# Optimization experiments

Measured on AMD Instinct MI355X. Metric: run time of the kernel, lower is better.

Reference implementation:

```python
import jax, jax.numpy as jnp
import numpy as np

B, H, W, C, HEADS = 32, 56, 56, 384, 12
WIN = (7, 7)
SHIFT = (3, 3)
N = WIN[0] * WIN[1]
HD = C // HEADS
HIDDEN = int(C * 2.0)
CPB_HIDDEN = 512


def _cpb_tables():
    # log-spaced continuous relative coordinates table (SwinV2 CPB)
    coords = [np.arange(-(w - 1), w, dtype=np.float32) for w in WIN]
    g = np.stack(np.meshgrid(*coords, indexing='ij'))
    for i, w in enumerate(WIN):
        g[i] = g[i] / (w - 1)
    rel = np.moveaxis(g, 0, -1)[None]              # (1, 2w0-1, 2w1-1, 2)
    rel = 8.0 * rel
    rel = np.sign(rel) * np.log2(np.abs(rel) + 1.0) / np.log2(8.0)
    grid = np.stack(np.meshgrid(*[np.arange(w) for w in WIN], indexing='ij')).reshape(2, -1)
    dists = grid[:, :, None] - grid[:, None, :]    # (2, N, N)
    dists[0] = (dists[0] + WIN[0] - 1) * (2 * WIN[1] - 1)
    dists[1] = (dists[1] + WIN[1] - 1)
    return jnp.asarray(rel, jnp.float32), jnp.asarray(dists.sum(0), jnp.int32)

REL_TAB, RPB_IDX = _cpb_tables()


def _compute_mask():
    img = np.zeros((1, H, W, 1), np.float32)
    cnt = 0
    for s0 in (slice(0, -WIN[0]), slice(-WIN[0], -SHIFT[0]), slice(-SHIFT[0], None)):
        for s1 in (slice(0, -WIN[1]), slice(-WIN[1], -SHIFT[1]), slice(-SHIFT[1], None)):
            img[:, s0, s1, :] = cnt
            cnt += 1
    w = img.reshape(1, H // WIN[0], WIN[0], W // WIN[1], WIN[1], 1)
    w = w.transpose(0, 1, 3, 2, 4, 5).reshape(-1, N)
    m = w[:, None, :] - w[:, :, None]
    return jnp.asarray(np.where(m != 0, -100.0, 0.0).astype(np.float32))


def _layernorm(x, g, b, eps=1e-5):
    mu = x.mean(-1, keepdims=True)
    var = ((x - mu) ** 2).mean(-1, keepdims=True)
    return (x - mu) / jnp.sqrt(var + eps) * g + b


def _window_partition(x):
    b = x.shape[0]
    x = x.reshape(b, H // WIN[0], WIN[0], W // WIN[1], WIN[1], C)
    return x.transpose(0, 1, 3, 2, 4, 5).reshape(-1, N, C)


def _window_reverse(win):
    x = win.reshape(B, H // WIN[0], W // WIN[1], WIN[0], WIN[1], C)
    return x.transpose(0, 1, 3, 2, 4, 5).reshape(B, H, W, C)


def setup_inputs() -> dict:
    key = jax.random.key(0)
    ks = jax.random.split(key, 16)
    s = 0.02
    return {
        'x': jax.random.normal(ks[0], (B, H, W, C), jnp.float32),
        'attn_mask': _compute_mask(),                              # (nW, N, N)
        'norm1_g': jnp.ones((C,), jnp.float32),
        'norm1_b': jnp.zeros((C,), jnp.float32),
        'qkv_w': jax.random.normal(ks[1], (3 * C, C), jnp.float32) * s,
        'qkv_b': jnp.zeros((3 * C,), jnp.float32),
        'proj_w': jax.random.normal(ks[2], (C, C), jnp.float32) * s,
        'proj_b': jnp.zeros((C,), jnp.float32),
        'cpb_w1': jax.random.normal(ks[3], (CPB_HIDDEN, 2), jnp.float32) * s,
        'cpb_b1': jnp.zeros((CPB_HIDDEN,), jnp.float32),
        'cpb_w2': jax.random.normal(ks[4], (HEADS, CPB_HIDDEN), jnp.float32) * s,
        'logit_scale': jnp.full((HEADS, 1, 1), np.log(10.0), jnp.float32),
        'norm2_g': jnp.ones((C,), jnp.float32),
        'norm2_b': jnp.zeros((C,), jnp.float32),
        'mlp_w1': jax.random.normal(ks[5], (HIDDEN, C), jnp.float32) * s,
        'mlp_b1': jnp.zeros((HIDDEN,), jnp.float32),
        'mlp_w2': jax.random.normal(ks[6], (C, HIDDEN), jnp.float32) * s,
        'mlp_b2': jnp.zeros((C,), jnp.float32),
    }


def reference(x, attn_mask, norm1_g, norm1_b, qkv_w, qkv_b, proj_w, proj_b,
              cpb_w1, cpb_b1, cpb_w2, logit_scale, norm2_g, norm2_b,
              mlp_w1, mlp_b1, mlp_w2, mlp_b2):
    # continuous position bias: MLP over log-spaced rel coords, gathered per pair
    h = jax.nn.relu(REL_TAB @ cpb_w1.T + cpb_b1)       # (1, 2w0-1, 2w1-1, 512)
    tab = (h @ cpb_w2.T).reshape(-1, HEADS)            # ((2w0-1)*(2w1-1), heads)
    rpb = tab[RPB_IDX.reshape(-1)].reshape(N, N, HEADS)
    rpb = 16.0 * jax.nn.sigmoid(rpb)
    rpb = rpb.transpose(2, 0, 1)                       # (heads, N, N)

    shortcut = x
    xn = _layernorm(x, norm1_g, norm1_b)
    xs = jnp.roll(xn, (-SHIFT[0], -SHIFT[1]), axis=(1, 2))
    wnd = _window_partition(xs)                        # (B*nW, N, C)
    qkv = (wnd @ qkv_w.T + qkv_b).reshape(-1, N, 3, HEADS, HD)
    q = qkv[:, :, 0].transpose(0, 2, 1, 3)             # (B*nW, heads, N, hd)
    k = qkv[:, :, 1].transpose(0, 2, 1, 3)
    v = qkv[:, :, 2].transpose(0, 2, 1, 3)
    qn = q / jnp.maximum(jnp.linalg.norm(q, axis=-1, keepdims=True), 1e-12)
    kn = k / jnp.maximum(jnp.linalg.norm(k, axis=-1, keepdims=True), 1e-12)
    scale = jnp.exp(jnp.minimum(logit_scale, jnp.log(100.0)))   # (heads,1,1)
    attn = jnp.einsum('bhnd,bhmd->bhnm', qn, kn) * scale + rpb
    nW = attn_mask.shape[0]
    attn = attn.reshape(B, nW, HEADS, N, N) + attn_mask[None, :, None]
    attn = jax.nn.softmax(attn.reshape(-1, HEADS, N, N), axis=-1)
    o = jnp.einsum('bhnm,bhmd->bhnd', attn, v)
    o = o.transpose(0, 2, 1, 3).reshape(-1, N, C)
    o = o @ proj_w.T + proj_b
    xr = _window_reverse(o)
    xr = jnp.roll(xr, (SHIFT[0], SHIFT[1]), axis=(1, 2))
    x = shortcut + xr
    xm = _layernorm(x, norm2_g, norm2_b)
    xm = jax.nn.gelu(xm @ mlp_w1.T + mlp_b1, approximate=False) @ mlp_w2.T + mlp_b2
    return x + xm
```

## Files before the change

kernel.cpp:

```cpp
#include <hip/hip_runtime.h>
#include <stdint.h>

typedef unsigned short u16;
typedef __bf16 bf16x8 __attribute__((ext_vector_type(8)));
typedef float f32x4 __attribute__((ext_vector_type(4)));

__device__ __forceinline__ float b2f(u16 u) {
    union { float f; uint32_t i; } x; x.i = ((uint32_t)u) << 16; return x.f;
}
__device__ __forceinline__ u16 f2b(float f) {
    union { float f; uint32_t i; } x; x.f = f;
    uint32_t r = (x.i + 0x7fffu + ((x.i >> 16) & 1u)) >> 16;
    return (u16)r;
}

__global__ __launch_bounds__(512)
void cpb_tab_kernel(const float* __restrict__ w1, const float* __restrict__ b1,
                    const float* __restrict__ w2, float* __restrict__ tab) {
    __shared__ float hbuf[512];
    int p = blockIdx.x, j = threadIdx.x;
    int i0 = p / 13, i1 = p % 13;
    float c0 = (i0 - 6) * (8.0f / 6.0f), c1 = (i1 - 6) * (8.0f / 6.0f);
    float r0 = copysignf(log2f(fabsf(c0) + 1.0f) * (1.0f / 3.0f), c0);
    float r1 = copysignf(log2f(fabsf(c1) + 1.0f) * (1.0f / 3.0f), c1);
    float h = r0 * w1[j * 2] + r1 * w1[j * 2 + 1] + b1[j];
    hbuf[j] = fmaxf(h, 0.0f);
    __syncthreads();
    if (j < 12) {
        float s = 0.0f;
        for (int t = 0; t < 512; t++) s += w2[j * 512 + t] * hbuf[t];
        tab[p * 12 + j] = s;
    }
}

__global__ __launch_bounds__(256)
void cpb_gather_kernel(const float* __restrict__ tab, float* __restrict__ rpb) {
    int idx = blockIdx.x * 256 + threadIdx.x;
    if (idx >= 12 * 2401) return;
    int h = idx / 2401, r = idx % 2401, i = r / 49, j = r % 49;
    int d = (i / 7 - j / 7 + 6) * 13 + (i % 7 - j % 7 + 6);
    float v = tab[d * 12 + h];
    rpb[idx] = 16.0f / (1.0f + expf(-v));
}

__global__ __launch_bounds__(256)
void wconv_kernel(const float* __restrict__ s0, const float* __restrict__ s1,
                  const float* __restrict__ s2, const float* __restrict__ s3,
                  u16* __restrict__ dst) {
    int i = (blockIdx.x * 256 + threadIdx.x) * 4;
    if (i >= 1179648) return;
    const float* src; int off;
    if (i < 442368)      { src = s0; off = i; }
    else if (i < 589824) { src = s1; off = i - 442368; }
    else if (i < 884736) { src = s2; off = i - 589824; }
    else                 { src = s3; off = i - 884736; }
    float4 v = *(const float4*)(src + off);
    u16 o[4] = {f2b(v.x), f2b(v.y), f2b(v.z), f2b(v.w)};
    *(uint2*)(dst + i) = *(const uint2*)o;
}

template <int PERM>
__global__ __launch_bounds__(256)
void ln_fused_kernel(const float* __restrict__ in, const float* __restrict__ g,
                     const float* __restrict__ b, u16* __restrict__ outb) {
    int wave = threadIdx.x >> 6, lane = threadIdx.x & 63;
    int tok = blockIdx.x * 4 + wave;
    size_t src = (size_t)tok * 384;
    float2 v[3];
    float s = 0.0f, s2 = 0.0f;
#pragma unroll
    for (int i = 0; i < 3; i++) {
        v[i] = *(const float2*)&in[src + i * 128 + lane * 2];
        s += v[i].x + v[i].y;
        s2 += v[i].x * v[i].x + v[i].y * v[i].y;
    }
#pragma unroll
    for (int m = 32; m >= 1; m >>= 1) { s += __shfl_xor(s, m, 64); s2 += __shfl_xor(s2, m, 64); }
    float mu = s * (1.0f / 384.0f);
    float rstd = rsqrtf(s2 * (1.0f / 384.0f) - mu * mu + 1e-5f);
    int drow = tok;
    if (PERM) {
        int bb = tok / 3136, rr = tok % 3136;
        int h = rr / 56, w = rr % 56;
        int hs = h - 3; if (hs < 0) hs += 56;
        int wsr = w - 3; if (wsr < 0) wsr += 56;
        int wi = (hs / 7) * 8 + (wsr / 7);
        int n = (hs % 7) * 7 + (wsr % 7);
        drow = (bb * 64 + wi) * 49 + n;
    }
    size_t dst = (size_t)drow * 384;
#pragma unroll
    for (int i = 0; i < 3; i++) {
        int c = i * 128 + lane * 2;
        float2 gg = *(const float2*)&g[c];
        float2 bv = *(const float2*)&b[c];
        u16 o[2] = { f2b((v[i].x - mu) * rstd * gg.x + bv.x),
                     f2b((v[i].y - mu) * rstd * gg.y + bv.y) };
        *(uint32_t*)&outb[dst + c] = *(const uint32_t*)o;
    }
}

enum { SRC_PLAIN = 0, SRC_HEADMAJ = 1 };
enum { EPI_QKV = 0, EPI_PROJ = 1, EPI_MLP1 = 2, EPI_MLP2 = 3 };
#define LDP 40

template <int SRC, int EPI>
__global__ __launch_bounds__(256)
void gemm_mfma(const u16* __restrict__ A, const u16* __restrict__ Wb,
               const float* __restrict__ bias, int K,
               u16* __restrict__ o0, u16* __restrict__ o1, u16* __restrict__ o2,
               const float* __restrict__ xres, float* __restrict__ dout) {
    const int tid = threadIdx.x;
    const int wave = tid >> 6, lane = tid & 63, quad = lane >> 4, l16 = lane & 15;
    const int wm = (wave >> 1) * 64, wn = (wave & 1) * 64;
    const int m0 = blockIdx.y * 128, n0 = blockIdx.x * 128;
    __shared__ alignas(16) u16 lA[128 * LDP];
    __shared__ alignas(16) u16 lB[128 * LDP];
    f32x4 acc[4][4] = {};

    size_t abase[2], wbase[2];
#pragma unroll
    for (int s = 0; s < 2; s++) {
        int row = (tid + s * 256) >> 2;
        int grow = m0 + row;
        if (SRC == SRC_HEADMAJ) {
            int widx = grow / 49, n = grow % 49;
            abase[s] = (size_t)widx * 18816 + (size_t)n * 32;
        } else {
            abase[s] = (size_t)grow * (size_t)K;
        }
        wbase[s] = (size_t)(n0 + row) * (size_t)K;
    }

    for (int kk = 0; kk < K; kk += 32) {
        __syncthreads();
#pragma unroll
        for (int s = 0; s < 2; s++) {
            int c = tid + s * 256;
            int row = c >> 2, seg = c & 3;
            size_t aoff = (SRC == SRC_HEADMAJ)
                              ? (size_t)(kk >> 5) * 1568 + seg * 8
                              : (size_t)kk + seg * 8;
            *(int4*)&lA[row * LDP + seg * 8] = *(const int4*)&A[abase[s] + aoff];
            *(int4*)&lB[row * LDP + seg * 8] = *(const int4*)&Wb[wbase[s] + kk + seg * 8];
        }
        __syncthreads();
        bf16x8 af[4], bfr[4];
#pragma unroll
        for (int t = 0; t < 4; t++)
            af[t] = *(const bf16x8*)&lA[(wm + t * 16 + l16) * LDP + quad * 8];
#pragma unroll
        for (int t = 0; t < 4; t++)
            bfr[t] = *(const bf16x8*)&lB[(wn + t * 16 + l16) * LDP + quad * 8];
#pragma unroll
        for (int i = 0; i < 4; i++)
#pragma unroll
            for (int j = 0; j < 4; j++)
                acc[i][j] = __builtin_amdgcn_mfma_f32_16x16x32_bf16(af[i], bfr[j], acc[i][j], 0, 0, 0);
    }

#pragma unroll
    for (int i = 0; i < 4; i++) {
#pragma unroll
        for (int r = 0; r < 4; r++) {
            int row = m0 + wm + i * 16 + quad * 4 + r;
            int widx = 0, n = 0;
            size_t pbase = 0;
            if (EPI == EPI_QKV || EPI == EPI_PROJ) { widx = row / 49; n = row % 49; }
            if (EPI == EPI_PROJ) {
                int bb = widx >> 6, wi = widx & 63;
                int hs = (wi >> 3) * 7 + n / 7, wsr = (wi & 7) * 7 + n % 7;
                int h = hs + 3; if (h >= 56) h -= 56;
                int w = wsr + 3; if (w >= 56) w -= 56;
                pbase = (((size_t)bb * 56 + h) * 56 + w) * 384;
            }
#pragma unroll
            for (int j = 0; j < 4; j++) {
                int col = n0 + wn + j * 16 + l16;
                float v = acc[i][j][r] + bias[col];
                if (EPI == EPI_QKV) {
                    int which = col / 384, head = (col >> 5) % 12, hd = col & 31;
                    u16* dst = (which == 0) ? o0 : ((which == 1) ? o1 : o2);
                    dst[(size_t)(widx * 12 + head) * 1568 + n * 32 + hd] = f2b(v);
                } else if (EPI == EPI_PROJ) {
                    dout[pbase + col] = v + xres[pbase + col];
                } else if (EPI == EPI_MLP1) {
                    float ge = 0.5f * v * (1.0f + erff(v * 0.70710678f));
                    o0[(size_t)row * 768 + col] = f2b(ge);
                } else {
                    size_t o = (size_t)row * 384 + col;
                    dout[o] = v + dout[o];
                }
            }
        }
    }
}

__global__ __launch_bounds__(256)
void attn_mfma_kernel(const u16* __restrict__ q, const u16* __restrict__ k,
                      const u16* __restrict__ v, const float* __restrict__ rpb,
                      const float* __restrict__ mask, const float* __restrict__ lsc,
                      u16* __restrict__ out) {
    __shared__ alignas(16) u16 sP[4][64 * 72];
    __shared__ alignas(16) u16 sVT[4][32 * 72];
    __shared__ float sQin[4][64], sKin[4][64];
    const int tid = threadIdx.x;
    const int wave = tid >> 6, lane = tid & 63;
    const int quad = lane >> 4, l16 = lane & 15;
    const int unit = blockIdx.x * 4 + wave;
    const int widx = unit / 12, head = unit - widx * 12;
    const size_t base = (size_t)unit * 1568;
    u16* pP  = sP[wave];
    u16* pVT = sVT[wave];
    float* qin = sQin[wave];
    float* kin = sKin[wave];

    if (lane >= 49) { qin[lane] = 0.0f; kin[lane] = 0.0f; }

    {
        const bool valid = lane < 49;
#pragma unroll
        for (int c = 0; c < 4; c++) {
            u16 r8[8] = {0, 0, 0, 0, 0, 0, 0, 0};
            if (valid) *(int4*)r8 = *(const int4*)&v[base + lane * 32 + c * 8];
#pragma unroll
            for (int e = 0; e < 8; e++) pVT[(c * 8 + e) * 72 + lane] = r8[e];
        }
    }

    const float lscale = __expf(fminf(lsc[head], 4.6051702f));
    bf16x8 qf[4], kf[4];
#pragma unroll
    for (int t = 0; t < 4; t++) {
        int row = t * 16 + l16; if (row > 48) row = 48;
        int4 qa = *(const int4*)&q[base + row * 32 + quad * 8];
        int4 ka = *(const int4*)&k[base + row * 32 + quad * 8];
        u16 qu[8], ku[8];
        *(int4*)qu = qa; *(int4*)ku = ka;
        float qs2 = 0.f, ks2 = 0.f;
#pragma unroll
        for (int e = 0; e < 8; e++) {
            float a = b2f(qu[e]), b = b2f(ku[e]);
            qs2 = fmaf(a, a, qs2); ks2 = fmaf(b, b, ks2);
        }
        qs2 += __shfl_xor(qs2, 16, 64); qs2 += __shfl_xor(qs2, 32, 64);
        ks2 += __shfl_xor(ks2, 16, 64); ks2 += __shfl_xor(ks2, 32, 64);
        if (quad == 0) {
            qin[row] = lscale * rsqrtf(fmaxf(qs2, 1e-24f));
            kin[row] = rsqrtf(fmaxf(ks2, 1e-24f));
        }
        qf[t] = *(bf16x8*)&qa;
        kf[t] = *(bf16x8*)&ka;
    }

    f32x4 s[4][4] = {};
#pragma unroll
    for (int mi = 0; mi < 4; mi++)
#pragma unroll
        for (int ni = 0; ni < 4; ni++)
            s[mi][ni] = __builtin_amdgcn_mfma_f32_16x16x32_bf16(qf[mi], kf[ni], s[mi][ni], 0, 0, 0);

    const float* rp = rpb + (size_t)head * 2401;
    const float* mk = mask + (size_t)(widx & 63) * 2401;
    float kj[4];
#pragma unroll
    for (int ni = 0; ni < 4; ni++) kj[ni] = kin[ni * 16 + l16];
#pragma unroll
    for (int mi = 0; mi < 4; mi++) {
#pragma unroll
        for (int r = 0; r < 4; r++) {
            const int i = mi * 16 + quad * 4 + r;
            const float qi = qin[i];
            const int ic = (i < 49 ? i : 48) * 49;
            const float* brow = rp + ic;
            const float* mrow = mk + ic;
            float lg[4];
#pragma unroll
            for (int ni = 0; ni < 4; ni++) {
                const int j = ni * 16 + l16;
                lg[ni] = (j < 49) ? fmaf(s[mi][ni][r], qi * kj[ni], brow[j] + mrow[j]) : -1e30f;
            }
            float m = fmaxf(fmaxf(lg[0], lg[1]), fmaxf(lg[2], lg[3]));
            m = fmaxf(m, __shfl_xor(m, 1, 64));
            m = fmaxf(m, __shfl_xor(m, 2, 64));
            m = fmaxf(m, __shfl_xor(m, 4, 64));
            m = fmaxf(m, __shfl_xor(m, 8, 64));
            float p0 = __expf(lg[0] - m), p1 = __expf(lg[1] - m);
            float p2 = __expf(lg[2] - m), p3 = __expf(lg[3] - m);
            float sum = p0 + p1 + p2 + p3;
            sum += __shfl_xor(sum, 1, 64);
            sum += __shfl_xor(sum, 2, 64);
            sum += __shfl_xor(sum, 4, 64);
            sum += __shfl_xor(sum, 8, 64);
            const float inv = 1.0f / sum;
            pP[i * 72 +  0 + l16] = f2b(p0 * inv);
            pP[i * 72 + 16 + l16] = f2b(p1 * inv);
            pP[i * 72 + 32 + l16] = f2b(p2 * inv);
            pP[i * 72 + 48 + l16] = f2b(p3 * inv);
        }
    }

    bf16x8 vf[2][2];
#pragma unroll
    for (int kk = 0; kk < 2; kk++)
#pragma unroll
        for (int ni = 0; ni < 2; ni++)
            vf[kk][ni] = *(const bf16x8*)&pVT[(ni * 16 + l16) * 72 + kk * 32 + quad * 8];
    f32x4 o[4][2] = {};
#pragma unroll
    for (int mi = 0; mi < 4; mi++)
#pragma unroll
        for (int kk = 0; kk < 2; kk++) {
            bf16x8 pa = *(const bf16x8*)&pP[(mi * 16 + l16) * 72 + kk * 32 + quad * 8];
#pragma unroll
            for (int ni = 0; ni < 2; ni++)
                o[mi][ni] = __builtin_amdgcn_mfma_f32_16x16x32_bf16(pa, vf[kk][ni], o[mi][ni], 0, 0, 0);
        }

#pragma unroll
    for (int mi = 0; mi < 4; mi++)
#pragma unroll
        for (int r = 0; r < 4; r++) {
            const int i = mi * 16 + quad * 4 + r;
            if (i < 49) {
                out[base + i * 32 + l16]      = f2b(o[mi][0][r]);
                out[base + i * 32 + 16 + l16] = f2b(o[mi][1][r]);
            }
        }
}

extern "C" void kernel_launch(void* const* d_in, const int* in_sizes, int n_in,
                              void* d_out, int out_size, void* d_ws, size_t ws_size,
                              hipStream_t stream) {
    const float* x      = (const float*)d_in[0];
    const float* mask   = (const float*)d_in[1];
    const float* n1g    = (const float*)d_in[2];
    const float* n1b    = (const float*)d_in[3];
    const float* qkv_w  = (const float*)d_in[4];
    const float* qkv_b  = (const float*)d_in[5];
    const float* proj_w = (const float*)d_in[6];
    const float* proj_b = (const float*)d_in[7];
    const float* cpb_w1 = (const float*)d_in[8];
    const float* cpb_b1 = (const float*)d_in[9];
    const float* cpb_w2 = (const float*)d_in[10];
    const float* lscale = (const float*)d_in[11];
    const float* n2g    = (const float*)d_in[12];
    const float* n2b    = (const float*)d_in[13];
    const float* mlp_w1 = (const float*)d_in[14];
    const float* mlp_b1 = (const float*)d_in[15];
    const float* mlp_w2 = (const float*)d_in[16];
    const float* mlp_b2 = (const float*)d_in[17];

    char* ws = (char*)d_ws;
    const size_t SLOT = 77070336ULL;
    float* tab = (float*)(ws);
    float* rpb = (float*)(ws + 16384);
    u16*  Wb   = (u16*)(ws + (1 << 20));
    u16*  qkv_wb  = Wb;
    u16*  proj_wb = Wb + 442368;
    u16*  mlp1_wb = Wb + 589824;
    u16*  mlp2_wb = Wb + 884736;
    u16* qb = (u16*)(ws + (4 << 20));
    u16* kb = (u16*)(ws + (4 << 20) + SLOT);
    u16* vb = (u16*)d_out;
    u16* xb = (u16*)((char*)d_out + SLOT);
    u16* attn_o = qb;
    u16* xb2    = kb;
    u16* hidden = qb;
    float* dout = (float*)d_out;

    wconv_kernel<<<1152, 256, 0, stream>>>(qkv_w, proj_w, mlp_w1, mlp_w2, Wb);
    cpb_tab_kernel<<<169, 512, 0, stream>>>(cpb_w1, cpb_b1, cpb_w2, tab);
    cpb_gather_kernel<<<113, 256, 0, stream>>>(tab, rpb);
    ln_fused_kernel<1><<<25088, 256, 0, stream>>>(x, n1g, n1b, xb);
    gemm_mfma<SRC_PLAIN, EPI_QKV><<<dim3(9, 784), 256, 0, stream>>>(
        xb, qkv_wb, qkv_b, 384, qb, kb, vb, nullptr, nullptr);
    attn_mfma_kernel<<<6144, 256, 0, stream>>>(qb, kb, vb, rpb, mask, lscale, attn_o);
    gemm_mfma<SRC_HEADMAJ, EPI_PROJ><<<dim3(3, 784), 256, 0, stream>>>(
        attn_o, proj_wb, proj_b, 384, nullptr, nullptr, nullptr, x, dout);
    ln_fused_kernel<0><<<25088, 256, 0, stream>>>(dout, n2g, n2b, xb2);
    for (int h = 0; h < 2; h++) {
        gemm_mfma<SRC_PLAIN, EPI_MLP1><<<dim3(6, 392), 256, 0, stream>>>(
            xb2 + (size_t)h * 50176 * 384, mlp1_wb, mlp_b1, 384,
            hidden, nullptr, nullptr, nullptr, nullptr);
        gemm_mfma<SRC_PLAIN, EPI_MLP2><<<dim3(3, 392), 256, 0, stream>>>(
            hidden, mlp2_wb, mlp_b2, 768, nullptr, nullptr, nullptr,
            nullptr, dout + (size_t)h * 50176 * 384);
    }
}
```

Baseline: 1.172 ms.

## Load GEMM tiles with direct global-to-LDS loads, XOR swizzle, and XCD block remap

Replaces the register-staged int4 copies in the MFMA GEMM with global_load_lds 16-byte direct loads into an unpadded LDS tile. It adds an XOR swizzle on the 16-byte column chunks to avoid bank conflicts in place of the old padding. It also switches to a 1D grid remapped so that consecutive blocks on the same XCD (bid&7) cover contiguous tiles, which should improve L2 reuse. The goal is to cut VGPR staging and instruction overhead in the load path. The risks are a fragile swizzle and grid-size divisibility assumptions (all grids are multiples of 8).

```diff
diff --git a/kernel.cpp b/kernel.cpp
--- a/kernel.cpp
+++ b/kernel.cpp
@@ -12,6 +12,10 @@
     union { float f; uint32_t i; } x; x.f = f;
     uint32_t r = (x.i + 0x7fffu + ((x.i >> 16) & 1u)) >> 16;
     return (u16)r;
+}
+__device__ __forceinline__ void gll16(const void* g, void* l) {
+    __builtin_amdgcn_global_load_lds((const __attribute__((address_space(1))) void*)g,
+                                     (__attribute__((address_space(3))) void*)l, 16, 0, 0);
 }
 
 __global__ __launch_bounds__(512)
@@ -102,9 +106,8 @@
 
 enum { SRC_PLAIN = 0, SRC_HEADMAJ = 1 };
 enum { EPI_QKV = 0, EPI_PROJ = 1, EPI_MLP1 = 2, EPI_MLP2 = 3 };
-#define LDP 40
-
-template <int SRC, int EPI>
+
+template <int SRC, int EPI, int GX>
 __global__ __launch_bounds__(256)
 void gemm_mfma(const u16* __restrict__ A, const u16* __restrict__ Wb,
                const float* __restrict__ bias, int K,
@@ -113,45 +116,52 @@
     const int tid = threadIdx.x;
     const int wave = tid >> 6, lane = tid & 63, quad = lane >> 4, l16 = lane & 15;
     const int wm = (wave >> 1) * 64, wn = (wave & 1) * 64;
-    const int m0 = blockIdx.y * 128, n0 = blockIdx.x * 128;
-    __shared__ alignas(16) u16 lA[128 * LDP];
-    __shared__ alignas(16) u16 lB[128 * LDP];
+    const int bid = blockIdx.x;
+    const int nb = (bid & 7) * ((int)gridDim.x >> 3) + (bid >> 3);
+    const int m0 = (nb / GX) * 128, n0 = (nb % GX) * 128;
+    __shared__ alignas(16) u16 lA[128 * 32];
+    __shared__ alignas(16) u16 lB[128 * 32];
     f32x4 acc[4][4] = {};
 
-    size_t abase[2], wbase[2];
+    const int c4 = lane & 3, rsub = lane >> 2;
+    size_t agb[2], wgb[2];
 #pragma unroll
     for (int s = 0; s < 2; s++) {
-        int row = (tid + s * 256) >> 2;
+        int row = (wave * 2 + s) * 16 + rsub;
+        int swz = (c4 ^ ((row >> 1) & 3)) * 16;
         int grow = m0 + row;
         if (SRC == SRC_HEADMAJ) {
             int widx = grow / 49, n = grow % 49;
-            abase[s] = (size_t)widx * 18816 + (size_t)n * 32;
+            agb[s] = ((size_t)widx * 18816 + (size_t)n * 32) * 2 + swz;
         } else {
-            abase[s] = (size_t)grow * (size_t)K;
-        }
-        wbase[s] = (size_t)(n0 + row) * (size_t)K;
-    }
+            agb[s] = (size_t)grow * (size_t)K * 2 + swz;
+        }
+        wgb[s] = (size_t)(n0 + row) * (size_t)K * 2 + swz;
+    }
+    const char* Ac = (const char*)A;
+    const char* Wc = (const char*)Wb;
+    char* ldsA = (char*)lA;
+    char* ldsB = (char*)lB;
+    const int swzR = (quad ^ ((l16 >> 1) & 3)) * 16;
 
     for (int kk = 0; kk < K; kk += 32) {
         __syncthreads();
-#pragma unroll
-        for (int s = 0; s < 2; s++) {
-            int c = tid + s * 256;
-            int row = c >> 2, seg = c & 3;
-            size_t aoff = (SRC == SRC_HEADMAJ)
-                              ? (size_t)(kk >> 5) * 1568 + seg * 8
-                              : (size_t)kk + seg * 8;
-            *(int4*)&lA[row * LDP + seg * 8] = *(const int4*)&A[abase[s] + aoff];
-            *(int4*)&lB[row * LDP + seg * 8] = *(const int4*)&Wb[wbase[s] + kk + seg * 8];
-        }
+        size_t ka = (SRC == SRC_HEADMAJ) ? (size_t)(kk >> 5) * 3136 : (size_t)kk * 2;
+        size_t kb = (size_t)kk * 2;
+#pragma unroll
+        for (int s = 0; s < 2; s++)
+            gll16(Ac + agb[s] + ka, ldsA + (wave * 2 + s) * 1024);
+#pragma unroll
+        for (int s = 0; s < 2; s++)
+            gll16(Wc + wgb[s] + kb, ldsB + (wave * 2 + s) * 1024);
         __syncthreads();
         bf16x8 af[4], bfr[4];
 #pragma unroll
         for (int t = 0; t < 4; t++)
-            af[t] = *(const bf16x8*)&lA[(wm + t * 16 + l16) * LDP + quad * 8];
+            af[t] = *(const bf16x8*)(ldsA + (wm + t * 16 + l16) * 64 + swzR);
 #pragma unroll
         for (int t = 0; t < 4; t++)
-            bfr[t] = *(const bf16x8*)&lB[(wn + t * 16 + l16) * LDP + quad * 8];
+            bfr[t] = *(const bf16x8*)(ldsB + (wn + t * 16 + l16) * 64 + swzR);
 #pragma unroll
         for (int i = 0; i < 4; i++)
 #pragma unroll
@@ -373,17 +383,17 @@
     cpb_tab_kernel<<<169, 512, 0, stream>>>(cpb_w1, cpb_b1, cpb_w2, tab);
     cpb_gather_kernel<<<113, 256, 0, stream>>>(tab, rpb);
     ln_fused_kernel<1><<<25088, 256, 0, stream>>>(x, n1g, n1b, xb);
-    gemm_mfma<SRC_PLAIN, EPI_QKV><<<dim3(9, 784), 256, 0, stream>>>(
+    gemm_mfma<SRC_PLAIN, EPI_QKV, 9><<<7056, 256, 0, stream>>>(
         xb, qkv_wb, qkv_b, 384, qb, kb, vb, nullptr, nullptr);
     attn_mfma_kernel<<<6144, 256, 0, stream>>>(qb, kb, vb, rpb, mask, lscale, attn_o);
-    gemm_mfma<SRC_HEADMAJ, EPI_PROJ><<<dim3(3, 784), 256, 0, stream>>>(
+    gemm_mfma<SRC_HEADMAJ, EPI_PROJ, 3><<<2352, 256, 0, stream>>>(
         attn_o, proj_wb, proj_b, 384, nullptr, nullptr, nullptr, x, dout);
     ln_fused_kernel<0><<<25088, 256, 0, stream>>>(dout, n2g, n2b, xb2);
     for (int h = 0; h < 2; h++) {
-        gemm_mfma<SRC_PLAIN, EPI_MLP1><<<dim3(6, 392), 256, 0, stream>>>(
+        gemm_mfma<SRC_PLAIN, EPI_MLP1, 6><<<2352, 256, 0, stream>>>(
             xb2 + (size_t)h * 50176 * 384, mlp1_wb, mlp_b1, 384,
             hidden, nullptr, nullptr, nullptr, nullptr);
-        gemm_mfma<SRC_PLAIN, EPI_MLP2><<<dim3(3, 392), 256, 0, stream>>>(
+        gemm_mfma<SRC_PLAIN, EPI_MLP2, 3><<<1176, 256, 0, stream>>>(
             hidden, mlp2_wb, mlp_b2, 768, nullptr, nullptr, nullptr,
             nullptr, dout + (size_t)h * 50176 * 384);
     }
```

New measurement: 1.118 ms. -4.6%, faster.
